# Kernel tuning notes

Hardware: AMD Instinct MI355X
Metric: run time of the kernel (lower is better)

## Reference

```python
import jax, jax.numpy as jnp
import numpy as np

N_NODES = 100000
N_EDGES = 1600000
IN_C, HID, OUT_C = 128, 128, 64
N_LAYERS = 4


def setup_inputs() -> dict:
    key = jax.random.key(0)
    ks = jax.random.split(key, 12)
    s_in = 1.0 / np.sqrt(IN_C)
    s_h = 1.0 / np.sqrt(HID)
    x = jax.random.normal(ks[0], (N_NODES, IN_C), dtype=jnp.float32)
    edge_index = jax.random.randint(ks[1], (2, N_EDGES), 0, N_NODES, dtype=jnp.int64)
    return {
        "x": x,
        "edge_index": edge_index,
        "W_in": jax.random.uniform(ks[2], (IN_C, HID), jnp.float32, -s_in, s_in),
        "b_in": jax.random.uniform(ks[3], (HID,), jnp.float32, -s_in, s_in),
        "W_conv": jax.random.uniform(ks[4], (N_LAYERS, HID, HID), jnp.float32, -s_h, s_h),
        "b_conv": jax.random.uniform(ks[5], (N_LAYERS, HID), jnp.float32, -s_h, s_h),
        "alpha": 0.1 * jax.random.normal(ks[6], (N_LAYERS,), jnp.float32),
        "beta": 1.0 + 0.1 * jax.random.normal(ks[7], (N_LAYERS,), jnp.float32),
        "W_out": jax.random.uniform(ks[8], (HID, OUT_C), jnp.float32, -s_h, s_h),
        "b_out": jax.random.uniform(ks[9], (OUT_C,), jnp.float32, -s_h, s_h),
    }


def _gcn_norm(edge_index, n_nodes):
    # add self-loops, symmetric deg^-1/2 normalization (PyG gcn_norm, edge_weight=1)
    loop = jnp.arange(n_nodes, dtype=edge_index.dtype)
    src = jnp.concatenate([edge_index[0], loop])
    dst = jnp.concatenate([edge_index[1], loop])
    deg = jax.ops.segment_sum(jnp.ones_like(dst, dtype=jnp.float32), dst, n_nodes)
    dinv = jnp.where(deg > 0, jax.lax.rsqrt(deg), 0.0)
    norm = dinv[src] * dinv[dst]  # [E + N]
    return src, dst, norm


def _gcn_conv(h, W, b, src, dst, norm, n_nodes):
    h = h @ W                                 # [N, HID]
    msg = h[src] * norm[:, None]              # gather + scale, [E+N, HID]
    agg = jax.ops.segment_sum(msg, dst, n_nodes)  # scatter-add back to nodes
    return agg + b


def reference(x, edge_index, W_in, b_in, W_conv, b_conv, alpha, beta, W_out, b_out):
    n = x.shape[0]
    src, dst, norm = _gcn_norm(edge_index, n)
    h = x @ W_in + b_in
    inp = h
    for i in range(N_LAYERS):
        h = _gcn_conv(inp, W_conv[i], b_conv[i], src, dst, norm, n)
        h = jnp.tanh(h)                        # activation='Tanh'; dropout p=0
        h = beta[i] * inp + alpha[i] * h       # rezero residual
        inp = h
    logits = h @ W_out + b_out
    return jax.nn.log_softmax(logits, axis=1)
```

## Files before the change

### kernel.cpp

```cpp
#include <hip/hip_runtime.h>
#include <cstdint>
#include <cstddef>


constexpr int K = 128;

typedef __bf16 bf16x8 __attribute__((ext_vector_type(8)));
typedef float f32x4 __attribute__((ext_vector_type(4)));
typedef float f32x2 __attribute__((ext_vector_type(2)));

__device__ inline uint16_t f2bf(float f) {
    union { float f; uint32_t u; } c; c.f = f;
    uint32_t r = (c.u + 0x7fffu + ((c.u >> 16) & 1u)) >> 16;
    return (uint16_t)r;
}
__device__ inline float blo(uint32_t u) { union { uint32_t i; float f; } c; c.i = u << 16; return c.f; }
__device__ inline float bhi(uint32_t u) { union { uint32_t i; float f; } c; c.i = u & 0xffff0000u; return c.f; }

__device__ inline float fast_tanh(float x) {
    union { float f; uint32_t u; } cx; cx.f = x;
    uint32_t sgn = cx.u & 0x80000000u;
    cx.u &= 0x7fffffffu;
    float t = __expf(2.0f * cx.f);
    float r = fmaf(-2.0f, __builtin_amdgcn_rcpf(t + 1.0f), 1.0f);
    union { float f; uint32_t u; } cr; cr.f = r;
    cr.u |= sgn;
    return cr.f;
}


__global__ __launch_bounds__(256) void s1_hist(const int* __restrict__ dst,
                                               int* __restrict__ ghist, int E) {
    __shared__ int hist[1024];
    for (int i = threadIdx.x; i < 1024; i += 256) hist[i] = 0;
    __syncthreads();
    int stride = gridDim.x * 256;
    for (int e = blockIdx.x * 256 + threadIdx.x; e < E; e += stride)
        atomicAdd(&hist[dst[e] >> 7], 1);
    __syncthreads();
    for (int i = threadIdx.x; i < 1024; i += 256) {
        int c = hist[i];
        if (c) atomicAdd(&ghist[i], c);
    }
}

__global__ void s2_scan(const int* __restrict__ ghist, int* __restrict__ gbase,
                        int* __restrict__ gcur, int* __restrict__ off, int N, int E) {
    __shared__ int buf[1024];
    int t = threadIdx.x;
    int v = ghist[t];
    buf[t] = v;
    __syncthreads();
    for (int o = 1; o < 1024; o <<= 1) {
        int add = (t >= o) ? buf[t - o] : 0;
        __syncthreads();
        buf[t] += add;
        __syncthreads();
    }
    int ex = buf[t] - v;
    gbase[t] = ex;
    gcur[t] = ex;
    if (t == 1023) gbase[1024] = buf[1023];
    if (t == 0) off[N] = E;
}

__global__ __launch_bounds__(256) void s3_scatter(
    const int* __restrict__ src, const int* __restrict__ dst,
    int* __restrict__ gcur, int* __restrict__ ebuf, int E)
{
    __shared__ int hist[1024], base[1024], cursor[1024];
    const int t = threadIdx.x;
    const int tile = blockIdx.x * 4096;
    for (int i = t; i < 1024; i += 256) { hist[i] = 0; cursor[i] = 0; }
    __syncthreads();
    int sv[16], dv[16];
#pragma unroll
    for (int k = 0; k < 16; ++k) {
        int e = tile + k * 256 + t;
        bool ok = e < E;
        sv[k] = ok ? src[e] : -1;
        dv[k] = ok ? dst[e] : 0;
        if (ok) atomicAdd(&hist[dv[k] >> 7], 1);
    }
    __syncthreads();
    for (int i = t; i < 1024; i += 256) {
        int c = hist[i];
        base[i] = c ? atomicAdd(&gcur[i], c) : 0;
    }
    __syncthreads();
#pragma unroll
    for (int k = 0; k < 16; ++k) {
        if (sv[k] >= 0) {
            int b = dv[k] >> 7;
            int r = atomicAdd(&cursor[b], 1);
            ebuf[base[b] + r] = (sv[k] << 7) | (dv[k] & 127);
        }
    }
}

__global__ __launch_bounds__(256) void s4_finalize(
    const int* __restrict__ gbase, const int* __restrict__ ebuf,
    int* __restrict__ csr, int* __restrict__ off, float* __restrict__ dinv,
    int N, int E)
{
    __shared__ int hist[128], excl[128], cursor[128];
    const int b = blockIdx.x;
    const int t = threadIdx.x;
    const int lo = gbase[b], hi = gbase[b + 1];
    if (t < 128) hist[t] = 0;
    __syncthreads();
    for (int i = lo + t; i < hi; i += 256) atomicAdd(&hist[ebuf[i] & 127], 1);
    __syncthreads();
    if (t < 128) excl[t] = hist[t];
    __syncthreads();
    for (int o = 1; o < 128; o <<= 1) {
        int v = (t < 128 && t >= o) ? excl[t - o] : 0;
        __syncthreads();
        if (t < 128) excl[t] += v;
        __syncthreads();
    }
    if (t < 128) {
        int node = b * 128 + t;
        int ex = excl[t] - hist[t];
        cursor[t] = ex;
        if (node < N) {
            off[node] = lo + ex;
            dinv[node] = rsqrtf((float)hist[t] + 1.0f);
        }
    }
    __syncthreads();
    for (int i = lo + t; i < hi; i += 256) {
        int v = ebuf[i];
        int r = atomicAdd(&cursor[v & 127], 1);
        csr[lo + r] = v & ~127;
    }
}


__global__ void wconv_all(const float* __restrict__ Win, const float* __restrict__ Wc,
                          const float* __restrict__ Wo, uint16_t* __restrict__ Tin,
                          uint16_t* __restrict__ Tc, uint16_t* __restrict__ To) {
    int idx = blockIdx.x * 256 + threadIdx.x;
    if (idx < 16384) {
        int c = idx >> 7, k = idx & 127;
        Tin[idx] = f2bf(Win[k * 128 + c]);
    } else if (idx < 81920) {
        int t = idx - 16384;
        int l = t >> 14, li = t & 16383;
        int c = li >> 7, k = li & 127;
        Tc[t] = f2bf(Wc[l * 16384 + k * 128 + c]);
    } else if (idx < 90112) {
        int t = idx - 81920;
        int c = t >> 7, k = t & 127;
        To[t] = f2bf(Wo[k * 64 + c]);
    }
}


template <int NOUT, bool A_FP32, int OMODE>
__global__ __launch_bounds__(256) void mfma_gemm(
    const void* __restrict__ Aptr, const uint16_t* __restrict__ Wt,
    const float* __restrict__ bias, float* __restrict__ outF,
    uint16_t* __restrict__ outB, uint8_t* __restrict__ outQ,
    const float* __restrict__ rowscale, int M)
{
    constexpr int NT = NOUT / 16;
    const int tid = threadIdx.x;
    const int w = tid >> 6;
    const int l = tid & 63;
    const int lg = l >> 4;
    const int lr = l & 15;
    const int rbase = blockIdx.x * 128 + w * 32;
    const int r0c = min(rbase + lr, M - 1);
    const int r1c = min(rbase + 16 + lr, M - 1);

    f32x4 acc[2][NT] = {};

    for (int k0 = 0; k0 < K; k0 += 32) {
        const int ka = k0 + lg * 8;
        bf16x8 a0, a1;
        if constexpr (A_FP32) {
            const float* A = (const float*)Aptr;
            const float* p0 = A + (size_t)r0c * K + ka;
            const float* p1 = A + (size_t)r1c * K + ka;
            float4 u0 = *(const float4*)p0, v0 = *(const float4*)(p0 + 4);
            float4 u1 = *(const float4*)p1, v1 = *(const float4*)(p1 + 4);
            a0[0] = (__bf16)u0.x; a0[1] = (__bf16)u0.y; a0[2] = (__bf16)u0.z; a0[3] = (__bf16)u0.w;
            a0[4] = (__bf16)v0.x; a0[5] = (__bf16)v0.y; a0[6] = (__bf16)v0.z; a0[7] = (__bf16)v0.w;
            a1[0] = (__bf16)u1.x; a1[1] = (__bf16)u1.y; a1[2] = (__bf16)u1.z; a1[3] = (__bf16)u1.w;
            a1[4] = (__bf16)v1.x; a1[5] = (__bf16)v1.y; a1[6] = (__bf16)v1.z; a1[7] = (__bf16)v1.w;
        } else {
            const uint16_t* A = (const uint16_t*)Aptr;
            a0 = *reinterpret_cast<const bf16x8*>(A + (size_t)r0c * K + ka);
            a1 = *reinterpret_cast<const bf16x8*>(A + (size_t)r1c * K + ka);
        }
#pragma unroll
        for (int ct = 0; ct < NT; ++ct) {
            bf16x8 b = *reinterpret_cast<const bf16x8*>(Wt + (size_t)(ct * 16 + lr) * K + ka);
            acc[0][ct] = __builtin_amdgcn_mfma_f32_16x16x32_bf16(a0, b, acc[0][ct], 0, 0, 0);
            acc[1][ct] = __builtin_amdgcn_mfma_f32_16x16x32_bf16(a1, b, acc[1][ct], 0, 0, 0);
        }
    }

    float bv[NT];
    if constexpr (OMODE == 0 || OMODE == 1) {
#pragma unroll
        for (int ct = 0; ct < NT; ++ct) bv[ct] = bias[ct * 16 + lr];
    }

    if constexpr (OMODE == 1) {
#pragma unroll
        for (int t = 0; t < 2; ++t) {
#pragma unroll
            for (int i = 0; i < 4; ++i) {
                float v[NT];
                float m = -3.0e38f;
#pragma unroll
                for (int ct = 0; ct < NT; ++ct) {
                    v[ct] = acc[t][ct][i] + bv[ct];
                    m = fmaxf(m, v[ct]);
                }
#pragma unroll
                for (int o = 8; o >= 1; o >>= 1) m = fmaxf(m, __shfl_xor(m, o));
                float s = 0.f;
#pragma unroll
                for (int ct = 0; ct < NT; ++ct) s += __expf(v[ct] - m);
#pragma unroll
                for (int o = 8; o >= 1; o >>= 1) s += __shfl_xor(s, o);
                float lse = m + __logf(s);
                int rr = rbase + t * 16 + lg * 4 + i;
                if (rr < M) {
#pragma unroll
                    for (int ct = 0; ct < NT; ++ct)
                        outF[(size_t)rr * NOUT + ct * 16 + lr] = v[ct] - lse;
                }
            }
        }
    } else {
#pragma unroll
        for (int t = 0; t < 2; ++t) {
#pragma unroll
            for (int i = 0; i < 4; ++i) {
                int rr = rbase + t * 16 + lg * 4 + i;
                if (rr < M) {
                    float sc = 1.0f;
                    if constexpr (OMODE == 2) sc = rowscale[rr];
#pragma unroll
                    for (int ct = 0; ct < NT; ++ct) {
                        float v = acc[t][ct][i];
                        size_t o = (size_t)rr * NOUT + ct * 16 + lr;
                        if constexpr (OMODE == 0) {
                            outB[o] = f2bf(v + bv[ct]);
                        } else {
                            v *= sc;
                            int pk = __builtin_amdgcn_cvt_pk_fp8_f32(v, v, 0, false);
                            outQ[o] = (uint8_t)(pk & 0xff);
                        }
                    }
                }
            }
        }
    }
}


__global__ __launch_bounds__(256) void agg_kernel(
    const uint8_t* __restrict__ B, uint16_t* __restrict__ A,
    const float* __restrict__ dinv, const int* __restrict__ off,
    const int* __restrict__ csr, const float* __restrict__ bconv,
    const float* __restrict__ alpha, const float* __restrict__ beta,
    int n, int E)
{
    int gid = blockIdx.x * 256 + threadIdx.x;
    int d = gid >> 6;
    int lane = threadIdx.x & 63;
    if (d >= n) return;

    const int half = lane >> 5;
    const int c0 = (lane & 31) * 4;
    f32x2 acc01 = {0.f, 0.f}, acc23 = {0.f, 0.f};
    const int s0 = off[d], s1 = off[d + 1];
    const int deg = s1 - s0;
    const int full = deg & ~63;

    for (int j0 = s0; j0 < s0 + full; j0 += 64) {
        int sv = csr[j0 + lane];
        for (int it = 0; it < 64; it += 16) {
            uint32_t u[8];
#pragma unroll
            for (int q = 0; q < 8; ++q) {
                int o = __shfl(sv, it + 2 * q + half);
                u[q] = *(const uint32_t*)(B + o + c0);
            }
#pragma unroll
            for (int q = 0; q < 8; ++q) {
                acc01 += __builtin_amdgcn_cvt_pk_f32_fp8((int)u[q], false);
                acc23 += __builtin_amdgcn_cvt_pk_f32_fp8((int)u[q], true);
            }
        }
    }
    int rem = deg - full;
    if (rem) {
        int idx = s0 + full + lane;
        int sv = csr[min(idx, E - 1)];
        for (int it = 0; it < rem; it += 16) {
            uint32_t u[8];
#pragma unroll
            for (int q = 0; q < 8; ++q) {
                int e = it + 2 * q + half;
                int o = __shfl(sv, e);
                u[q] = (e < rem) ? *(const uint32_t*)(B + o + c0) : 0u;
            }
#pragma unroll
            for (int q = 0; q < 8; ++q) {
                acc01 += __builtin_amdgcn_cvt_pk_f32_fp8((int)u[q], false);
                acc23 += __builtin_amdgcn_cvt_pk_f32_fp8((int)u[q], true);
            }
        }
    }
    {
        uint32_t u = *(const uint32_t*)(B + ((size_t)d << 7) + c0);
        acc01 += __builtin_amdgcn_cvt_pk_f32_fp8((int)u, false);
        acc23 += __builtin_amdgcn_cvt_pk_f32_fp8((int)u, true);
    }
    float a0 = acc01[0], a1 = acc01[1], a2 = acc23[0], a3 = acc23[1];
    a0 += __shfl_xor(a0, 32); a1 += __shfl_xor(a1, 32);
    a2 += __shfl_xor(a2, 32); a3 += __shfl_xor(a3, 32);

    float dd = dinv[d];
    float al = alpha[0], be = beta[0];
    float4 bb = *(const float4*)(bconv + c0);
    uint2 ip = *(const uint2*)(A + (size_t)d * K + c0);
    float o0 = be * blo(ip.x) + al * fast_tanh(fmaf(dd, a0, bb.x));
    float o1 = be * bhi(ip.x) + al * fast_tanh(fmaf(dd, a1, bb.y));
    float o2 = be * blo(ip.y) + al * fast_tanh(fmaf(dd, a2, bb.z));
    float o3 = be * bhi(ip.y) + al * fast_tanh(fmaf(dd, a3, bb.w));
    if (half == 0) {
        uint2 pk;
        asm("v_cvt_pk_bf16_f32 %0, %1, %2" : "=v"(pk.x) : "v"(o0), "v"(o1));
        asm("v_cvt_pk_bf16_f32 %0, %1, %2" : "=v"(pk.y) : "v"(o2), "v"(o3));
        *(uint2*)(A + (size_t)d * K + c0) = pk;
    }
}


extern "C" void kernel_launch(void* const* d_in, const int* in_sizes, int n_in,
                              void* d_out, int out_size, void* d_ws, size_t ws_size,
                              hipStream_t stream)
{
    const float* x      = (const float*)d_in[0];
    const int*   ei     = (const int*)d_in[1];
    const float* W_in   = (const float*)d_in[2];
    const float* b_in   = (const float*)d_in[3];
    const float* W_conv = (const float*)d_in[4];
    const float* b_conv = (const float*)d_in[5];
    const float* alpha  = (const float*)d_in[6];
    const float* beta   = (const float*)d_in[7];
    const float* W_out  = (const float*)d_in[8];
    const float* b_out  = (const float*)d_in[9];
    float* out = (float*)d_out;

    const int N = in_sizes[0] / K;
    const int E = in_sizes[1] / 2;
    const int L = in_sizes[6];

    const int* src = ei;
    const int* dst = ei + E;

    char* p = (char*)d_ws;
    uint16_t* Abf = (uint16_t*)p;      p += (size_t)N * K * sizeof(uint16_t);
    uint8_t* Bq8 = (uint8_t*)p;        p += (size_t)N * K * sizeof(uint8_t);
    uint16_t* Wt_in = (uint16_t*)p;    p += (size_t)K * K * sizeof(uint16_t);
    uint16_t* Wt_conv = (uint16_t*)p;  p += (size_t)4 * K * K * sizeof(uint16_t);
    uint16_t* Wt_out = (uint16_t*)p;   p += (size_t)64 * K * sizeof(uint16_t);
    float* dinv = (float*)p;           p += (size_t)N * sizeof(float);
    int* off = (int*)p;                p += (size_t)(N + 1) * sizeof(int);
    int* csr = (int*)p;                p += (size_t)E * sizeof(int);
    int* ghist = (int*)p;              p += 1024 * sizeof(int);
    int* gbase = (int*)p;              p += 1025 * sizeof(int);
    int* gcur = (int*)p;               p += 1024 * sizeof(int);
    int* ebuf = (int*)p;               p += (size_t)E * sizeof(int);

    hipMemsetAsync(ghist, 0, 1024 * sizeof(int), stream);
    s1_hist<<<256, 256, 0, stream>>>(dst, ghist, E);
    s2_scan<<<1, 1024, 0, stream>>>(ghist, gbase, gcur, off, N, E);
    s3_scatter<<<(E + 4095) / 4096, 256, 0, stream>>>(src, dst, gcur, ebuf, E);
    s4_finalize<<<(N + 127) / 128, 256, 0, stream>>>(gbase, ebuf, csr, off, dinv, N, E);

    wconv_all<<<(90112 + 255) / 256, 256, 0, stream>>>(
        W_in, W_conv, W_out, Wt_in, Wt_conv, Wt_out);

    const int gblocks = (N + 127) / 128;
    mfma_gemm<128, true, 0><<<gblocks, 256, 0, stream>>>(
        x, Wt_in, b_in, nullptr, Abf, nullptr, nullptr, N);
    for (int l = 0; l < L; ++l) {
        mfma_gemm<128, false, 2><<<gblocks, 256, 0, stream>>>(
            Abf, Wt_conv + (size_t)l * K * K, nullptr, nullptr, nullptr, Bq8, dinv, N);
        agg_kernel<<<(N * 64 + 255) / 256, 256, 0, stream>>>(
            Bq8, Abf, dinv, off, csr, b_conv + (size_t)l * K,
            alpha + l, beta + l, N, E);
    }
    mfma_gemm<64, false, 1><<<gblocks, 256, 0, stream>>>(
        Abf, Wt_out, b_out, out, nullptr, nullptr, nullptr, N);
}
```

Before: 498.2 us.

## Rewrite aggregation edge loop with readlane offsets and a zero sentinel row

```diff
diff --git a/kernel.cpp b/kernel.cpp
--- a/kernel.cpp
+++ b/kernel.cpp
@@ -139,7 +139,8 @@
 
 __global__ void wconv_all(const float* __restrict__ Win, const float* __restrict__ Wc,
                           const float* __restrict__ Wo, uint16_t* __restrict__ Tin,
-                          uint16_t* __restrict__ Tc, uint16_t* __restrict__ To) {
+                          uint16_t* __restrict__ Tc, uint16_t* __restrict__ To,
+                          uint8_t* __restrict__ Bq8, int N) {
     int idx = blockIdx.x * 256 + threadIdx.x;
     if (idx < 16384) {
         int c = idx >> 7, k = idx & 127;
@@ -153,6 +154,8 @@
         int t = idx - 81920;
         int c = t >> 7, k = t & 127;
         To[t] = f2bf(Wo[k * 64 + c]);
+    } else if (idx < 90144) {
+        ((uint32_t*)(Bq8 + (size_t)N * 128))[idx - 90112] = 0u;
     }
 }
 
@@ -276,46 +279,26 @@
     int lane = threadIdx.x & 63;
     if (d >= n) return;
 
-    const int half = lane >> 5;
+    const bool half = (lane >> 5) != 0;
     const int c0 = (lane & 31) * 4;
+    const int zoff = n << 7;
     f32x2 acc01 = {0.f, 0.f}, acc23 = {0.f, 0.f};
-    const int s0 = off[d], s1 = off[d + 1];
-    const int deg = s1 - s0;
-    const int full = deg & ~63;
-
-    for (int j0 = s0; j0 < s0 + full; j0 += 64) {
-        int sv = csr[j0 + lane];
-        for (int it = 0; it < 64; it += 16) {
-            uint32_t u[8];
-#pragma unroll
-            for (int q = 0; q < 8; ++q) {
-                int o = __shfl(sv, it + 2 * q + half);
-                u[q] = *(const uint32_t*)(B + o + c0);
-            }
-#pragma unroll
-            for (int q = 0; q < 8; ++q) {
-                acc01 += __builtin_amdgcn_cvt_pk_f32_fp8((int)u[q], false);
-                acc23 += __builtin_amdgcn_cvt_pk_f32_fp8((int)u[q], true);
-            }
-        }
-    }
-    int rem = deg - full;
-    if (rem) {
-        int idx = s0 + full + lane;
+    const int s0 = __builtin_amdgcn_readfirstlane(off[d]);
+    const int s1 = __builtin_amdgcn_readfirstlane(off[d + 1]);
+
+    for (int j0 = s0; j0 < s1; j0 += 64) {
+        int idx = j0 + lane;
         int sv = csr[min(idx, E - 1)];
-        for (int it = 0; it < rem; it += 16) {
-            uint32_t u[8];
-#pragma unroll
-            for (int q = 0; q < 8; ++q) {
-                int e = it + 2 * q + half;
-                int o = __shfl(sv, e);
-                u[q] = (e < rem) ? *(const uint32_t*)(B + o + c0) : 0u;
-            }
-#pragma unroll
-            for (int q = 0; q < 8; ++q) {
-                acc01 += __builtin_amdgcn_cvt_pk_f32_fp8((int)u[q], false);
-                acc23 += __builtin_amdgcn_cvt_pk_f32_fp8((int)u[q], true);
-            }
+        sv = (idx < s1) ? sv : zoff;
+        const int cnt = min(64, s1 - j0);
+#pragma unroll 4
+        for (int e = 0; e < cnt; e += 2) {
+            int sA = __builtin_amdgcn_readlane(sv, e);
+            int sB = __builtin_amdgcn_readlane(sv, e + 1);
+            int dlt = half ? (sB - sA) : 0;
+            uint32_t u = *(const uint32_t*)(B + sA + (c0 + dlt));
+            acc01 += __builtin_amdgcn_cvt_pk_f32_fp8((int)u, false);
+            acc23 += __builtin_amdgcn_cvt_pk_f32_fp8((int)u, true);
         }
     }
     {
@@ -326,6 +309,13 @@
     float a0 = acc01[0], a1 = acc01[1], a2 = acc23[0], a3 = acc23[1];
     a0 += __shfl_xor(a0, 32); a1 += __shfl_xor(a1, 32);
     a2 += __shfl_xor(a2, 32); a3 += __shfl_xor(a3, 32);
+
+    {
+        uint32_t u = *(const uint32_t*)(B + ((size_t)d << 7) + c0);
+        f32x2 lo = __builtin_amdgcn_cvt_pk_f32_fp8((int)u, false);
+        f32x2 hi = __builtin_amdgcn_cvt_pk_f32_fp8((int)u, true);
+        a0 -= lo[0]; a1 -= lo[1]; a2 -= hi[0]; a3 -= hi[1];
+    }
 
     float dd = dinv[d];
     float al = alpha[0], be = beta[0];
@@ -335,7 +325,7 @@
     float o1 = be * bhi(ip.x) + al * fast_tanh(fmaf(dd, a1, bb.y));
     float o2 = be * blo(ip.y) + al * fast_tanh(fmaf(dd, a2, bb.z));
     float o3 = be * bhi(ip.y) + al * fast_tanh(fmaf(dd, a3, bb.w));
-    if (half == 0) {
+    if (!half) {
         uint2 pk;
         asm("v_cvt_pk_bf16_f32 %0, %1, %2" : "=v"(pk.x) : "v"(o0), "v"(o1));
         asm("v_cvt_pk_bf16_f32 %0, %1, %2" : "=v"(pk.y) : "v"(o2), "v"(o3));
@@ -369,7 +359,8 @@
 
     char* p = (char*)d_ws;
     uint16_t* Abf = (uint16_t*)p;      p += (size_t)N * K * sizeof(uint16_t);
-    uint8_t* Bq8 = (uint8_t*)p;        p += (size_t)N * K * sizeof(uint8_t);
+    uint8_t* Bq8 = (uint8_t*)p;        p += (size_t)(N + 1) * K * sizeof(uint8_t);
+    p = (char*)(((uintptr_t)p + 15) & ~(uintptr_t)15);
     uint16_t* Wt_in = (uint16_t*)p;    p += (size_t)K * K * sizeof(uint16_t);
     uint16_t* Wt_conv = (uint16_t*)p;  p += (size_t)4 * K * K * sizeof(uint16_t);
     uint16_t* Wt_out = (uint16_t*)p;   p += (size_t)64 * K * sizeof(uint16_t);
@@ -387,8 +378,8 @@
     s3_scatter<<<(E + 4095) / 4096, 256, 0, stream>>>(src, dst, gcur, ebuf, E);
     s4_finalize<<<(N + 127) / 128, 256, 0, stream>>>(gbase, ebuf, csr, off, dinv, N, E);
 
-    wconv_all<<<(90112 + 255) / 256, 256, 0, stream>>>(
-        W_in, W_conv, W_out, Wt_in, Wt_conv, Wt_out);
+    wconv_all<<<(90144 + 255) / 256, 256, 0, stream>>>(
+        W_in, W_conv, W_out, Wt_in, Wt_conv, Wt_out, Bq8, N);
 
     const int gblocks = (N + 127) / 128;
     mfma_gemm<128, true, 0><<<gblocks, 256, 0, stream>>>(
```

New measurement: 602.4 us. 20.9% more time.
